# Kernel tuning notes

Hardware: AMD Instinct MI355X
Metric: run time of the kernel (lower is better)

The kernel has to match this reference:

```python
import jax, jax.numpy as jnp
import numpy as np

N, E, R, H = 50000, 800000, 8, 1  # nodes, edges, relations, heads
IN_DIM = HID = OUT = 128
NEG_SLOPE = 0.2  # PyG RGATConv default


def _rgat_layer(x, W, q, k, b, src, dst, etype):
    """One RGATConv (additive-self-attention, across-relation softmax, dim=1).
    x: [N, Cin]; W: [R, Cin, H*C]; q,k: [H*C, H]; b: [H*C]."""
    n = x.shape[0]
    xr = jnp.einsum('nc,rcd->rnd', x, W)            # [R, N, H*C] per-relation transform
    qproj = jnp.einsum('rnd,dh->rnh', xr, q)        # [R, N, H]
    kproj = jnp.einsum('rnd,dh->rnh', xr, k)        # [R, N, H]
    out_j = xr[etype, src]                          # [E, H*C] transformed source feats
    alpha = jax.nn.leaky_relu(qproj[etype, dst] + kproj[etype, src], NEG_SLOPE)  # [E, H]
    # per-destination-node softmax over incoming edges (across relations)
    amax = jax.ops.segment_max(alpha, dst, num_segments=n)
    amax = jnp.where(jnp.isfinite(amax), amax, 0.0)
    ex = jnp.exp(alpha - amax[dst])                 # [E, H]
    denom = jax.ops.segment_sum(ex, dst, num_segments=n)
    alpha = ex / (denom[dst] + 1e-16)
    d = out_j.shape[1]
    c = d // H
    msg = (alpha[:, :, None] * out_j.reshape(-1, H, c)).reshape(-1, d)  # [E, H*C]
    out = jax.ops.segment_sum(msg, dst, num_segments=n)                  # [N, H*C]
    return out + b


def setup_inputs() -> dict:
    key = jax.random.key(0)
    ks = jax.random.split(key, 16)
    inp = {
        'x': jax.random.normal(ks[0], (N, IN_DIM), dtype=jnp.float32),
        'edge_index': jax.random.randint(ks[1], (2, E), 0, N, dtype=jnp.int32),
        'edge_type': jax.random.randint(ks[2], (E,), 0, R, dtype=jnp.int32),
    }
    dims = [(IN_DIM, HID), (HID, HID), (HID, OUT)]
    for i, (cin, cout) in enumerate(dims):
        d = H * cout
        s = 1.0 / np.sqrt(cin)
        inp[f'W{i}'] = jax.random.normal(ks[3 + 4 * i], (R, cin, d), dtype=jnp.float32) * s
        inp[f'q{i}'] = jax.random.normal(ks[4 + 4 * i], (d, H), dtype=jnp.float32) * (1.0 / np.sqrt(d))
        inp[f'k{i}'] = jax.random.normal(ks[5 + 4 * i], (d, H), dtype=jnp.float32) * (1.0 / np.sqrt(d))
        inp[f'b{i}'] = jnp.zeros((d,), dtype=jnp.float32)
    return inp


def reference(x, edge_index, edge_type, W0, q0, k0, b0, W1, q1, k1, b1, W2, q2, k2, b2):
    src, dst = edge_index[0], edge_index[1]
    h = jax.nn.relu(_rgat_layer(x, W0, q0, k0, b0, src, dst, edge_type))
    h = jax.nn.relu(_rgat_layer(h, W1, q1, k1, b1, src, dst, edge_type))
    return _rgat_layer(h, W2, q2, k2, b2, src, dst, edge_type)
```

## Files before the change

### kernel.cpp

```cpp
#include <hip/hip_runtime.h>
#include <hip/hip_bf16.h>
#include <cstdint>
#include <cstddef>

#define NNODES 50000
#define NEDGES 800000
#define NREL 8
#define DIM 128
#define KDIM (NREL * DIM)
#define NEG_SLOPE 0.2f

typedef __attribute__((ext_vector_type(8))) short short8;
typedef __attribute__((ext_vector_type(4))) float f32x4;


__global__ void k_hist(const int* __restrict__ ei, const int* __restrict__ et,
                       int* __restrict__ cnt, int E) {
  int e = blockIdx.x * 256 + threadIdx.x;
  if (e < E) {
    int d = ei[E + e];
    int t = et[e];
    atomicAdd(&cnt[d * NREL + t], 1);
  }
}

__global__ void k_scan_reduce(const int* __restrict__ cnt, int* __restrict__ sums, int n) {
  __shared__ int sd[256];
  int base = blockIdx.x * 4096;
  int t = threadIdx.x;
  int acc = 0;
  for (int i = t; i < 4096; i += 256) {
    int idx = base + i;
    if (idx < n) acc += cnt[idx];
  }
  sd[t] = acc; __syncthreads();
  for (int s = 128; s > 0; s >>= 1) {
    if (t < s) sd[t] += sd[t + s];
    __syncthreads();
  }
  if (t == 0) sums[blockIdx.x] = sd[0];
}

__global__ void k_scan_top(int* sums, int nb) {
  if (threadIdx.x == 0 && blockIdx.x == 0) {
    int run = 0;
    for (int i = 0; i < nb; i++) { int v = sums[i]; sums[i] = run; run += v; }
  }
}

__global__ void k_scan_final(const int* __restrict__ cnt, const int* __restrict__ sums,
                             int* __restrict__ offs, int n, int E) {
  __shared__ int sd[256];
  int base = blockIdx.x * 4096;
  int t = threadIdx.x;
  int run = sums[blockIdx.x];
  for (int c = 0; c < 16; c++) {
    int idx = base + c * 256 + t;
    int v = (idx < n) ? cnt[idx] : 0;
    sd[t] = v; __syncthreads();
    for (int s = 1; s < 256; s <<= 1) {
      int u = (t >= s) ? sd[t - s] : 0;
      __syncthreads();
      sd[t] += u;
      __syncthreads();
    }
    if (idx < n) offs[idx] = run + sd[t] - v;
    run += sd[255];
    __syncthreads();
  }
  if (blockIdx.x == 0 && t == 0) offs[n] = E;
}

__global__ void k_scatter(const int* __restrict__ ei, const int* __restrict__ et,
                          int* __restrict__ cursor, int* __restrict__ pk, int E) {
  int e = blockIdx.x * 256 + threadIdx.x;
  if (e < E) {
    int s = ei[e];
    int d = ei[E + e];
    int t = et[e];
    int pos = atomicAdd(&cursor[d * NREL + t], 1);
    pk[pos] = s | (t << 16);
  }
}


__global__ void k_splitW(const float* __restrict__ W, __hip_bfloat16* __restrict__ wht,
                         __hip_bfloat16* __restrict__ wlt) {
  int id = blockIdx.x * 256 + threadIdx.x;
  if (id >= KDIM * DIM) return;
  int k = id >> 7, n = id & 127;
  float v = W[id];
  __hip_bfloat16 h = __float2bfloat16(v);
  float hv = __bfloat162float(h);
  wht[(size_t)n * KDIM + k] = h;
  wlt[(size_t)n * KDIM + k] = __float2bfloat16(v - hv);
}

__global__ void k_wqk(const float* __restrict__ W, const float* __restrict__ q,
                      const float* __restrict__ k, float* __restrict__ wq,
                      float* __restrict__ wk) {
  int id = blockIdx.x * 256 + threadIdx.x;
  if (id >= 2 * NREL * DIM) return;
  int which = id >> 10;
  int rc = id & 1023;
  const float* wrow = W + (size_t)rc * DIM;
  const float* v = which ? k : q;
  float acc = 0.f;
#pragma unroll 8
  for (int d = 0; d < DIM; d++) acc += wrow[d] * v[d];
  (which ? wk : wq)[rc] = acc;
}

__global__ void k_qk(const float* __restrict__ x, const float* __restrict__ wq,
                     const float* __restrict__ wk, float* __restrict__ qp,
                     float* __restrict__ kp, int N) {
  int wid = (blockIdx.x * blockDim.x + threadIdx.x) >> 6;
  int lane = threadIdx.x & 63;
  if (wid >= N) return;
  float x0 = x[(size_t)wid * DIM + lane];
  float x1 = x[(size_t)wid * DIM + 64 + lane];
#pragma unroll
  for (int r = 0; r < NREL; r++) {
    float aq = x0 * wq[r * DIM + lane] + x1 * wq[r * DIM + 64 + lane];
    float ak = x0 * wk[r * DIM + lane] + x1 * wk[r * DIM + 64 + lane];
    for (int s = 32; s > 0; s >>= 1) {
      aq += __shfl_xor(aq, s);
      ak += __shfl_xor(ak, s);
    }
    if (lane == 0) {
      qp[(size_t)wid * NREL + r] = aq;
      kp[(size_t)wid * NREL + r] = ak;
    }
  }
}

__global__ void k_agg(const float* __restrict__ x, const float* __restrict__ qp,
                      const float* __restrict__ kp, const int* __restrict__ offs,
                      const int* __restrict__ pk, __hip_bfloat16* __restrict__ sbh,
                      __hip_bfloat16* __restrict__ sbl, int N) {
  int wid = (blockIdx.x * blockDim.x + threadIdx.x) >> 6;
  int lane = threadIdx.x & 63;
  if (wid >= N) return;
  int base = wid * NREL;
  int start = offs[base], end = offs[base + NREL];
  __hip_bfloat16* sh = sbh + (size_t)wid * KDIM;
  __hip_bfloat16* sl = sbl + (size_t)wid * KDIM;
  __hip_bfloat16 z = __float2bfloat16(0.f);
  if (start == end) {
#pragma unroll
    for (int r = 0; r < NREL; r++) {
      sh[r * DIM + lane] = z;       sh[r * DIM + 64 + lane] = z;
      sl[r * DIM + lane] = z;       sl[r * DIM + 64 + lane] = z;
    }
    return;
  }
  float m = -1e30f;
  for (int i = start + lane; i < end; i += 64) {
    int p = pk[i];
    int src = p & 0xffff, t = p >> 16;
    float a = qp[base + t] + kp[src * NREL + t];
    a = (a > 0.f) ? a : NEG_SLOPE * a;
    m = fmaxf(m, a);
  }
  for (int sft = 32; sft > 0; sft >>= 1) m = fmaxf(m, __shfl_xor(m, sft));
  float ssum = 0.f;
  for (int i = start + lane; i < end; i += 64) {
    int p = pk[i];
    int src = p & 0xffff, t = p >> 16;
    float a = qp[base + t] + kp[src * NREL + t];
    a = (a > 0.f) ? a : NEG_SLOPE * a;
    ssum += expf(a - m);
  }
  for (int sft = 32; sft > 0; sft >>= 1) ssum += __shfl_xor(ssum, sft);
  float inv = 1.f / (ssum + 1e-16f);
#pragma unroll
  for (int r = 0; r < NREL; r++) {
    int e0 = offs[base + r], e1 = offs[base + r + 1];
    float qv = qp[base + r];
    float a0 = 0.f, a1 = 0.f;
    for (int i = e0; i < e1; ++i) {
      int p = pk[i];
      int src = p & 0xffff;
      float a = qv + kp[src * NREL + r];
      a = (a > 0.f) ? a : NEG_SLOPE * a;
      float wgt = expf(a - m) * inv;
      a0 += wgt * x[(size_t)src * DIM + lane];
      a1 += wgt * x[(size_t)src * DIM + 64 + lane];
    }
    {
      __hip_bfloat16 h0 = __float2bfloat16(a0);
      sh[r * DIM + lane] = h0;
      sl[r * DIM + lane] = __float2bfloat16(a0 - __bfloat162float(h0));
      __hip_bfloat16 h1 = __float2bfloat16(a1);
      sh[r * DIM + 64 + lane] = h1;
      sl[r * DIM + 64 + lane] = __float2bfloat16(a1 - __bfloat162float(h1));
    }
  }
}

#define GM 64
#define ROWB 80

__global__ __launch_bounds__(256, 3) void k_gemm_mfma(
    const __hip_bfloat16* __restrict__ Ah, const __hip_bfloat16* __restrict__ Al,
    const __hip_bfloat16* __restrict__ Wh, const __hip_bfloat16* __restrict__ Wl,
    const float* __restrict__ bias, float* __restrict__ out, int M, int relu) {
  __shared__ char sAh[GM * ROWB], sAl[GM * ROWB];
  __shared__ char sWh[DIM * ROWB], sWl[DIM * ROWB];
  int t = threadIdx.x;
  int w = t >> 6, l = t & 63;
  int m0 = blockIdx.x * GM;

  f32x4 acc[4][2];
  f32x4 zero = {0.f, 0.f, 0.f, 0.f};
#pragma unroll
  for (int mt = 0; mt < 4; mt++)
#pragma unroll
    for (int nt = 0; nt < 2; nt++) acc[mt][nt] = zero;

  int srow = t >> 2;
  int sseg = t & 3;

  for (int k0 = 0; k0 < KDIM; k0 += 32) {
    {
      int m = m0 + srow;
      float4 vh = make_float4(0.f, 0.f, 0.f, 0.f), vl = vh;
      if (m < M) {
        const char* ph = (const char*)Ah + (size_t)m * 2048 + k0 * 2 + sseg * 16;
        const char* pl = (const char*)Al + (size_t)m * 2048 + k0 * 2 + sseg * 16;
        vh = *(const float4*)ph;
        vl = *(const float4*)pl;
      }
      *(float4*)(sAh + srow * ROWB + sseg * 16) = vh;
      *(float4*)(sAl + srow * ROWB + sseg * 16) = vl;
    }
#pragma unroll
    for (int rr = 0; rr < 2; rr++) {
      int n = srow + rr * 64;
      const char* ph = (const char*)Wh + (size_t)n * 2048 + k0 * 2 + sseg * 16;
      const char* pl = (const char*)Wl + (size_t)n * 2048 + k0 * 2 + sseg * 16;
      float4 vh = *(const float4*)ph;
      float4 vl = *(const float4*)pl;
      *(float4*)(sWh + n * ROWB + sseg * 16) = vh;
      *(float4*)(sWl + n * ROWB + sseg * 16) = vl;
    }
    __syncthreads();
    int kseg = (l >> 4) * 16;
    int r16 = l & 15;
    short8 fwh[2], fwl[2], fsh[4], fsl[4];
#pragma unroll
    for (int nt = 0; nt < 2; nt++) {
      int n = w * 32 + nt * 16 + r16;
      fwh[nt] = *(const short8*)(sWh + n * ROWB + kseg);
      fwl[nt] = *(const short8*)(sWl + n * ROWB + kseg);
    }
#pragma unroll
    for (int mt = 0; mt < 4; mt++) {
      int m = mt * 16 + r16;
      fsh[mt] = *(const short8*)(sAh + m * ROWB + kseg);
      fsl[mt] = *(const short8*)(sAl + m * ROWB + kseg);
    }
#pragma unroll
    for (int mt = 0; mt < 4; mt++)
#pragma unroll
      for (int nt = 0; nt < 2; nt++) {
        acc[mt][nt] = __builtin_amdgcn_mfma_f32_16x16x32_bf16(fwh[nt], fsh[mt], acc[mt][nt], 0, 0, 0);
        acc[mt][nt] = __builtin_amdgcn_mfma_f32_16x16x32_bf16(fwh[nt], fsl[mt], acc[mt][nt], 0, 0, 0);
        acc[mt][nt] = __builtin_amdgcn_mfma_f32_16x16x32_bf16(fwl[nt], fsh[mt], acc[mt][nt], 0, 0, 0);
      }
    __syncthreads();
  }
  int r16 = l & 15, rh = l >> 4;
#pragma unroll
  for (int mt = 0; mt < 4; mt++) {
    int m = m0 + mt * 16 + r16;
    if (m >= M) continue;
#pragma unroll
    for (int nt = 0; nt < 2; nt++) {
      int n = w * 32 + nt * 16 + rh * 4;
      float4 bv = *(const float4*)(bias + n);
      f32x4 a = acc[mt][nt];
      float4 o;
      o.x = a.x + bv.x; o.y = a.y + bv.y; o.z = a.z + bv.z; o.w = a.w + bv.w;
      if (relu) {
        o.x = fmaxf(o.x, 0.f); o.y = fmaxf(o.y, 0.f);
        o.z = fmaxf(o.z, 0.f); o.w = fmaxf(o.w, 0.f);
      }
      *(float4*)(out + (size_t)m * DIM + n) = o;
    }
  }
}


extern "C" void kernel_launch(void* const* d_in, const int* in_sizes, int n_in,
                              void* d_out, int out_size, void* d_ws, size_t ws_size,
                              hipStream_t stream) {
  const float* x = (const float*)d_in[0];
  const int* ei = (const int*)d_in[1];
  const int* et = (const int*)d_in[2];
  const float* Wl3[3] = {(const float*)d_in[3], (const float*)d_in[7], (const float*)d_in[11]};
  const float* ql[3] = {(const float*)d_in[4], (const float*)d_in[8], (const float*)d_in[12]};
  const float* kl[3] = {(const float*)d_in[5], (const float*)d_in[9], (const float*)d_in[13]};
  const float* bl[3] = {(const float*)d_in[6], (const float*)d_in[10], (const float*)d_in[14]};
  float* out = (float*)d_out;

  char* w = (char*)d_ws;
  auto alloc = [&](size_t bytes) -> char* {
    char* p = w;
    w += (bytes + 255) & ~(size_t)255;
    return p;
  };
  const int NK = NNODES * NREL;
  int* cnt = (int*)alloc((size_t)NK * 4);
  int* offs = (int*)alloc((size_t)(NK + 1) * 4);
  int* cursor = (int*)alloc((size_t)NK * 4);
  int* sums = (int*)alloc(256 * 4);
  int* pk = (int*)alloc((size_t)NEDGES * 4);
  float* wq = (float*)alloc((size_t)NREL * DIM * 4);
  float* wk = (float*)alloc((size_t)NREL * DIM * 4);
  float* qp = (float*)alloc((size_t)NNODES * NREL * 4);
  float* kp = (float*)alloc((size_t)NNODES * NREL * 4);
  __hip_bfloat16* sbh = (__hip_bfloat16*)alloc((size_t)NNODES * KDIM * 2);
  __hip_bfloat16* sbl = (__hip_bfloat16*)alloc((size_t)NNODES * KDIM * 2);
  __hip_bfloat16* wht = (__hip_bfloat16*)alloc((size_t)DIM * KDIM * 2);
  __hip_bfloat16* wlt = (__hip_bfloat16*)alloc((size_t)DIM * KDIM * 2);
  float* h1 = (float*)alloc((size_t)NNODES * DIM * 4);
  float* h2 = (float*)alloc((size_t)NNODES * DIM * 4);

  hipMemsetAsync(cnt, 0, (size_t)NK * 4, stream);
  k_hist<<<(NEDGES + 255) / 256, 256, 0, stream>>>(ei, et, cnt, NEDGES);
  int nchunk = (NK + 4095) / 4096;
  k_scan_reduce<<<nchunk, 256, 0, stream>>>(cnt, sums, NK);
  k_scan_top<<<1, 64, 0, stream>>>(sums, nchunk);
  k_scan_final<<<nchunk, 256, 0, stream>>>(cnt, sums, offs, NK, NEDGES);
  hipMemcpyAsync(cursor, offs, (size_t)NK * 4, hipMemcpyDeviceToDevice, stream);
  k_scatter<<<(NEDGES + 255) / 256, 256, 0, stream>>>(ei, et, cursor, pk, NEDGES);

  const float* hin = x;
  float* houts[3] = {h1, h2, out};
  for (int l = 0; l < 3; l++) {
    k_splitW<<<(KDIM * DIM + 255) / 256, 256, 0, stream>>>(Wl3[l], wht, wlt);
    k_wqk<<<(2 * NREL * DIM + 255) / 256, 256, 0, stream>>>(Wl3[l], ql[l], kl[l], wq, wk);
    k_qk<<<(NNODES + 3) / 4, 256, 0, stream>>>(hin, wq, wk, qp, kp, NNODES);
    k_agg<<<(NNODES + 3) / 4, 256, 0, stream>>>(hin, qp, kp, offs, pk, sbh, sbl, NNODES);
    k_gemm_mfma<<<(NNODES + GM - 1) / GM, 256, 0, stream>>>(sbh, sbl, wht, wlt, bl[l],
                                                            houts[l], NNODES, l < 2 ? 1 : 0);
    hin = houts[l];
  }
}
```

Before: 976.3 us.

## Fuse edge aggregation into MFMA GEMM and precompute softmax weights

Softmax weights are now computed once per edge in a separate k_alpha kernel and stored. A fused kernel gathers weighted neighbor features per relation into LDS as hi/lo bf16 and feeds them straight to MFMA. This removes the large N×1024 bf16 intermediate buffers and their global round trip. W is pre-swizzled into MFMA fragment order so it is read directly from global memory without LDS staging. The cost is serial per-node gathers inside the GEMM block, which may lower parallelism, plus an extra edge-weight array.

```diff
diff --git a/kernel.cpp b/kernel.cpp
--- a/kernel.cpp
+++ b/kernel.cpp
@@ -12,6 +12,17 @@
 
 typedef __attribute__((ext_vector_type(8))) short short8;
 typedef __attribute__((ext_vector_type(4))) float f32x4;
+
+static __device__ __forceinline__ short f2bf(float v) {
+  union { float f; unsigned u; } c; c.f = v;
+  unsigned u = c.u;
+  unsigned r = (u + 0x7fffu + ((u >> 16) & 1u)) >> 16;
+  return (short)r;
+}
+static __device__ __forceinline__ float bf2f(short s) {
+  union { unsigned u; float f; } c; c.u = ((unsigned)(unsigned short)s) << 16;
+  return c.f;
+}
 
 
 __global__ void k_hist(const int* __restrict__ ei, const int* __restrict__ et,
@@ -84,16 +95,26 @@
 }
 
 
-__global__ void k_splitW(const float* __restrict__ W, __hip_bfloat16* __restrict__ wht,
-                         __hip_bfloat16* __restrict__ wlt) {
+__global__ void k_splitW_frag(const float* __restrict__ W, short* __restrict__ Wfh,
+                              short* __restrict__ Wfl) {
   int id = blockIdx.x * 256 + threadIdx.x;
-  if (id >= KDIM * DIM) return;
-  int k = id >> 7, n = id & 127;
-  float v = W[id];
-  __hip_bfloat16 h = __float2bfloat16(v);
-  float hv = __bfloat162float(h);
-  wht[(size_t)n * KDIM + k] = h;
-  wlt[(size_t)n * KDIM + k] = __float2bfloat16(v - hv);
+  if (id >= 16384) return;
+  int l = id & 63;
+  int ng = (id >> 6) & 7;
+  int kc = (id >> 9) & 3;
+  int r = id >> 11;
+  int n = ng * 16 + (l & 15);
+  int k0 = r * 128 + kc * 32 + (l >> 4) * 8;
+  short8 vh, vl;
+#pragma unroll
+  for (int j = 0; j < 8; j++) {
+    float v = W[(size_t)(k0 + j) * DIM + n];
+    short h = f2bf(v);
+    vh[j] = h;
+    vl[j] = f2bf(v - bf2f(h));
+  }
+  ((short8*)Wfh)[id] = vh;
+  ((short8*)Wfl)[id] = vl;
 }
 
 __global__ void k_wqk(const float* __restrict__ W, const float* __restrict__ q,
@@ -134,26 +155,15 @@
   }
 }
 
-__global__ void k_agg(const float* __restrict__ x, const float* __restrict__ qp,
-                      const float* __restrict__ kp, const int* __restrict__ offs,
-                      const int* __restrict__ pk, __hip_bfloat16* __restrict__ sbh,
-                      __hip_bfloat16* __restrict__ sbl, int N) {
+__global__ void k_alpha(const float* __restrict__ qp, const float* __restrict__ kp,
+                        const int* __restrict__ offs, const int* __restrict__ pk,
+                        float* __restrict__ wgt, int N) {
   int wid = (blockIdx.x * blockDim.x + threadIdx.x) >> 6;
   int lane = threadIdx.x & 63;
   if (wid >= N) return;
   int base = wid * NREL;
   int start = offs[base], end = offs[base + NREL];
-  __hip_bfloat16* sh = sbh + (size_t)wid * KDIM;
-  __hip_bfloat16* sl = sbl + (size_t)wid * KDIM;
-  __hip_bfloat16 z = __float2bfloat16(0.f);
-  if (start == end) {
-#pragma unroll
-    for (int r = 0; r < NREL; r++) {
-      sh[r * DIM + lane] = z;       sh[r * DIM + 64 + lane] = z;
-      sl[r * DIM + lane] = z;       sl[r * DIM + 64 + lane] = z;
-    }
-    return;
-  }
+  if (start == end) return;
   float m = -1e30f;
   for (int i = start + lane; i < end; i += 64) {
     int p = pk[i];
@@ -162,54 +172,34 @@
     a = (a > 0.f) ? a : NEG_SLOPE * a;
     m = fmaxf(m, a);
   }
-  for (int sft = 32; sft > 0; sft >>= 1) m = fmaxf(m, __shfl_xor(m, sft));
+  for (int s = 32; s > 0; s >>= 1) m = fmaxf(m, __shfl_xor(m, s));
   float ssum = 0.f;
   for (int i = start + lane; i < end; i += 64) {
     int p = pk[i];
     int src = p & 0xffff, t = p >> 16;
     float a = qp[base + t] + kp[src * NREL + t];
     a = (a > 0.f) ? a : NEG_SLOPE * a;
-    ssum += expf(a - m);
-  }
-  for (int sft = 32; sft > 0; sft >>= 1) ssum += __shfl_xor(ssum, sft);
+    float e = expf(a - m);
+    wgt[i] = e;
+    ssum += e;
+  }
+  for (int s = 32; s > 0; s >>= 1) ssum += __shfl_xor(ssum, s);
   float inv = 1.f / (ssum + 1e-16f);
-#pragma unroll
-  for (int r = 0; r < NREL; r++) {
-    int e0 = offs[base + r], e1 = offs[base + r + 1];
-    float qv = qp[base + r];
-    float a0 = 0.f, a1 = 0.f;
-    for (int i = e0; i < e1; ++i) {
-      int p = pk[i];
-      int src = p & 0xffff;
-      float a = qv + kp[src * NREL + r];
-      a = (a > 0.f) ? a : NEG_SLOPE * a;
-      float wgt = expf(a - m) * inv;
-      a0 += wgt * x[(size_t)src * DIM + lane];
-      a1 += wgt * x[(size_t)src * DIM + 64 + lane];
-    }
-    {
-      __hip_bfloat16 h0 = __float2bfloat16(a0);
-      sh[r * DIM + lane] = h0;
-      sl[r * DIM + lane] = __float2bfloat16(a0 - __bfloat162float(h0));
-      __hip_bfloat16 h1 = __float2bfloat16(a1);
-      sh[r * DIM + 64 + lane] = h1;
-      sl[r * DIM + 64 + lane] = __float2bfloat16(a1 - __bfloat162float(h1));
-    }
-  }
-}
-
-#define GM 64
-#define ROWB 80
-
-__global__ __launch_bounds__(256, 3) void k_gemm_mfma(
-    const __hip_bfloat16* __restrict__ Ah, const __hip_bfloat16* __restrict__ Al,
-    const __hip_bfloat16* __restrict__ Wh, const __hip_bfloat16* __restrict__ Wl,
+  for (int i = start + lane; i < end; i += 64) wgt[i] *= inv;
+}
+
+#define PITCH 272
+
+__global__ __launch_bounds__(256, 4) void k_fused(
+    const float* __restrict__ x, const int* __restrict__ offs,
+    const int* __restrict__ pk, const float* __restrict__ wgt,
+    const short* __restrict__ Wfh, const short* __restrict__ Wfl,
     const float* __restrict__ bias, float* __restrict__ out, int M, int relu) {
-  __shared__ char sAh[GM * ROWB], sAl[GM * ROWB];
-  __shared__ char sWh[DIM * ROWB], sWl[DIM * ROWB];
+  __shared__ char sSh[64 * PITCH];
+  __shared__ char sSl[64 * PITCH];
   int t = threadIdx.x;
   int w = t >> 6, l = t & 63;
-  int m0 = blockIdx.x * GM;
+  int m0 = blockIdx.x * 64;
 
   f32x4 acc[4][2];
   f32x4 zero = {0.f, 0.f, 0.f, 0.f};
@@ -218,66 +208,69 @@
 #pragma unroll
     for (int nt = 0; nt < 2; nt++) acc[mt][nt] = zero;
 
-  int srow = t >> 2;
-  int sseg = t & 3;
-
-  for (int k0 = 0; k0 < KDIM; k0 += 32) {
-    {
-      int m = m0 + srow;
-      float4 vh = make_float4(0.f, 0.f, 0.f, 0.f), vl = vh;
-      if (m < M) {
-        const char* ph = (const char*)Ah + (size_t)m * 2048 + k0 * 2 + sseg * 16;
-        const char* pl = (const char*)Al + (size_t)m * 2048 + k0 * 2 + sseg * 16;
-        vh = *(const float4*)ph;
-        vl = *(const float4*)pl;
+  int nrow = w * 16;
+  const char* wfh_base = (const char*)Wfh + ((size_t)(w * 2) * 64 + l) * 16;
+  const char* wfl_base = (const char*)Wfl + ((size_t)(w * 2) * 64 + l) * 16;
+  int r16 = l & 15, hi16 = l >> 4;
+
+  for (int r = 0; r < NREL; r++) {
+    for (int nn = 0; nn < 16; nn++) {
+      int row = nrow + nn;
+      int node = m0 + row;
+      float a0 = 0.f, a1 = 0.f;
+      if (node < M) {
+        int e0 = offs[node * NREL + r];
+        int e1 = offs[node * NREL + r + 1];
+        for (int i = e0; i < e1; i++) {
+          int src = pk[i] & 0xffff;
+          float wg = wgt[i];
+          float2 xv = ((const float2*)(x + (size_t)src * DIM))[l];
+          a0 = fmaf(wg, xv.x, a0);
+          a1 = fmaf(wg, xv.y, a1);
+        }
       }
-      *(float4*)(sAh + srow * ROWB + sseg * 16) = vh;
-      *(float4*)(sAl + srow * ROWB + sseg * 16) = vl;
-    }
-#pragma unroll
-    for (int rr = 0; rr < 2; rr++) {
-      int n = srow + rr * 64;
-      const char* ph = (const char*)Wh + (size_t)n * 2048 + k0 * 2 + sseg * 16;
-      const char* pl = (const char*)Wl + (size_t)n * 2048 + k0 * 2 + sseg * 16;
-      float4 vh = *(const float4*)ph;
-      float4 vl = *(const float4*)pl;
-      *(float4*)(sWh + n * ROWB + sseg * 16) = vh;
-      *(float4*)(sWl + n * ROWB + sseg * 16) = vl;
+      short h0 = f2bf(a0), h1 = f2bf(a1);
+      short l0 = f2bf(a0 - bf2f(h0)), l1 = f2bf(a1 - bf2f(h1));
+      *(unsigned*)(sSh + row * PITCH + l * 4) =
+          (unsigned)(unsigned short)h0 | ((unsigned)(unsigned short)h1 << 16);
+      *(unsigned*)(sSl + row * PITCH + l * 4) =
+          (unsigned)(unsigned short)l0 | ((unsigned)(unsigned short)l1 << 16);
     }
     __syncthreads();
-    int kseg = (l >> 4) * 16;
-    int r16 = l & 15;
-    short8 fwh[2], fwl[2], fsh[4], fsl[4];
-#pragma unroll
-    for (int nt = 0; nt < 2; nt++) {
-      int n = w * 32 + nt * 16 + r16;
-      fwh[nt] = *(const short8*)(sWh + n * ROWB + kseg);
-      fwl[nt] = *(const short8*)(sWl + n * ROWB + kseg);
-    }
-#pragma unroll
-    for (int mt = 0; mt < 4; mt++) {
-      int m = mt * 16 + r16;
-      fsh[mt] = *(const short8*)(sAh + m * ROWB + kseg);
-      fsl[mt] = *(const short8*)(sAl + m * ROWB + kseg);
-    }
-#pragma unroll
-    for (int mt = 0; mt < 4; mt++)
+#pragma unroll
+    for (int kc = 0; kc < 4; kc++) {
+      size_t wfoff = (size_t)((r * 4 + kc) * 8) * 1024;
+      short8 fwh[2], fwl[2];
 #pragma unroll
       for (int nt = 0; nt < 2; nt++) {
-        acc[mt][nt] = __builtin_amdgcn_mfma_f32_16x16x32_bf16(fwh[nt], fsh[mt], acc[mt][nt], 0, 0, 0);
-        acc[mt][nt] = __builtin_amdgcn_mfma_f32_16x16x32_bf16(fwh[nt], fsl[mt], acc[mt][nt], 0, 0, 0);
-        acc[mt][nt] = __builtin_amdgcn_mfma_f32_16x16x32_bf16(fwl[nt], fsh[mt], acc[mt][nt], 0, 0, 0);
+        fwh[nt] = *(const short8*)(wfh_base + wfoff + (size_t)nt * 1024);
+        fwl[nt] = *(const short8*)(wfl_base + wfoff + (size_t)nt * 1024);
       }
+      short8 fsh[4], fsl[4];
+#pragma unroll
+      for (int mt = 0; mt < 4; mt++) {
+        int off = (mt * 16 + r16) * PITCH + kc * 64 + hi16 * 16;
+        fsh[mt] = *(const short8*)(sSh + off);
+        fsl[mt] = *(const short8*)(sSl + off);
+      }
+#pragma unroll
+      for (int mt = 0; mt < 4; mt++)
+#pragma unroll
+        for (int nt = 0; nt < 2; nt++) {
+          acc[mt][nt] = __builtin_amdgcn_mfma_f32_16x16x32_bf16(fwh[nt], fsh[mt], acc[mt][nt], 0, 0, 0);
+          acc[mt][nt] = __builtin_amdgcn_mfma_f32_16x16x32_bf16(fwh[nt], fsl[mt], acc[mt][nt], 0, 0, 0);
+          acc[mt][nt] = __builtin_amdgcn_mfma_f32_16x16x32_bf16(fwl[nt], fsh[mt], acc[mt][nt], 0, 0, 0);
+        }
+    }
     __syncthreads();
   }
-  int r16 = l & 15, rh = l >> 4;
 #pragma unroll
   for (int mt = 0; mt < 4; mt++) {
     int m = m0 + mt * 16 + r16;
     if (m >= M) continue;
 #pragma unroll
     for (int nt = 0; nt < 2; nt++) {
-      int n = w * 32 + nt * 16 + rh * 4;
+      int n = w * 32 + nt * 16 + hi16 * 4;
       float4 bv = *(const float4*)(bias + n);
       f32x4 a = acc[mt][nt];
       float4 o;
@@ -320,10 +313,9 @@
   float* wk = (float*)alloc((size_t)NREL * DIM * 4);
   float* qp = (float*)alloc((size_t)NNODES * NREL * 4);
   float* kp = (float*)alloc((size_t)NNODES * NREL * 4);
-  __hip_bfloat16* sbh = (__hip_bfloat16*)alloc((size_t)NNODES * KDIM * 2);
-  __hip_bfloat16* sbl = (__hip_bfloat16*)alloc((size_t)NNODES * KDIM * 2);
-  __hip_bfloat16* wht = (__hip_bfloat16*)alloc((size_t)DIM * KDIM * 2);
-  __hip_bfloat16* wlt = (__hip_bfloat16*)alloc((size_t)DIM * KDIM * 2);
+  float* wgt = (float*)alloc((size_t)NEDGES * 4);
+  short* Wfh = (short*)alloc((size_t)KDIM * DIM * 2);
+  short* Wfl = (short*)alloc((size_t)KDIM * DIM * 2);
   float* h1 = (float*)alloc((size_t)NNODES * DIM * 4);
   float* h2 = (float*)alloc((size_t)NNODES * DIM * 4);
 
@@ -339,12 +331,12 @@
   const float* hin = x;
   float* houts[3] = {h1, h2, out};
   for (int l = 0; l < 3; l++) {
-    k_splitW<<<(KDIM * DIM + 255) / 256, 256, 0, stream>>>(Wl3[l], wht, wlt);
+    k_splitW_frag<<<64, 256, 0, stream>>>(Wl3[l], Wfh, Wfl);
     k_wqk<<<(2 * NREL * DIM + 255) / 256, 256, 0, stream>>>(Wl3[l], ql[l], kl[l], wq, wk);
     k_qk<<<(NNODES + 3) / 4, 256, 0, stream>>>(hin, wq, wk, qp, kp, NNODES);
-    k_agg<<<(NNODES + 3) / 4, 256, 0, stream>>>(hin, qp, kp, offs, pk, sbh, sbl, NNODES);
-    k_gemm_mfma<<<(NNODES + GM - 1) / GM, 256, 0, stream>>>(sbh, sbl, wht, wlt, bl[l],
-                                                            houts[l], NNODES, l < 2 ? 1 : 0);
+    k_alpha<<<(NNODES + 3) / 4, 256, 0, stream>>>(qp, kp, offs, pk, wgt, NNODES);
+    k_fused<<<(NNODES + 63) / 64, 256, 0, stream>>>(hin, offs, pk, wgt, Wfh, Wfl,
+                                                    bl[l], houts[l], NNODES, l < 2 ? 1 : 0);
     hin = houts[l];
   }
 }
```

Measured after the change: 1.181 ms. 1.21x slower.
